# Optimization experiments

Measured on AMD Instinct MI355X. Metric: run time of the kernel, lower is better.

## Reference

```python
import jax, jax.numpy as jnp
import numpy as np

EPS = 1e-6


def _make_window_masks(nhw, nww, ws, shift):
    ph = jnp.arange(nhw).reshape(nhw, 1, 1, 1, 1, 1)
    pw = jnp.arange(nww).reshape(1, nww, 1, 1, 1, 1)
    qh = jnp.arange(ws).reshape(1, 1, ws, 1, 1, 1)
    qw = jnp.arange(ws).reshape(1, 1, 1, ws, 1, 1)
    kh = jnp.arange(ws).reshape(1, 1, 1, 1, ws, 1)
    kw = jnp.arange(ws).reshape(1, 1, 1, 1, 1, ws)
    top = ph == 0
    left = pw == 0
    qa = qh < shift
    ka = kh < shift
    ql = qw < shift
    kl = kw < shift
    m = ((left & top & (ql == kl) & (qa == ka))
         | (left & ~top & (ql == kl))
         | (~left & top & (qa == ka))
         | (~left & ~top))
    m = jnp.broadcast_to(m, (nhw, nww, ws, ws, ws, ws))
    return m.reshape(nhw, nww, ws * ws, ws * ws)


def _window(ws, x):
    # x: [b, nh, H, W, e] -> [b, nh, H//ws, W//ws, ws, ws, e]
    b, nh, H, W, e = x.shape
    x = x.reshape(b, nh, H // ws, ws, W // ws, ws, e)
    return jnp.transpose(x, (0, 1, 2, 4, 3, 5, 6))


def _unwindow(x):
    b, nh, h, w, wh, ww, e = x.shape
    x = jnp.transpose(x, (0, 1, 2, 4, 3, 5, 6))
    return x.reshape(b, nh, h * wh, w * ww, e)


def _rope_theta(pos, n_heads, d_head):
    # AxialRoPE: dim = d_head // 2, freqs [n_heads, dim//4]
    dim = d_head // 2
    freqs = jnp.exp(jnp.linspace(np.float32(np.log(np.pi)), np.float32(np.log(10.0 * np.pi)), n_heads * dim // 4 + 1)[:-1])
    freqs = freqs.reshape(dim // 4, n_heads).T  # [nh, dim//4]
    th = pos[..., None, 0:1] * freqs  # [b,H,W,nh,dim//4]
    tw = pos[..., None, 1:2] * freqs
    theta = jnp.concatenate([th, tw], axis=-1)  # [b,H,W,nh,d_head//4]
    return jnp.moveaxis(theta, -2, -4)  # [b,nh,H,W,d_head//4]


def _apply_rope(x, theta):
    # rotates first 2*d of head dim, pairs (i, i+d); rest passes through
    d = theta.shape[-1]
    x1, x2, rest = x[..., :d], x[..., d:2 * d], x[..., 2 * d:]
    cos, sin = jnp.cos(theta), jnp.sin(theta)
    y1 = x1 * cos - x2 * sin
    y2 = x2 * cos + x1 * sin
    return jnp.concatenate([y1, y2, rest], axis=-1)


def _forward(x, pos, cond, norm_scale, mod_w, mod_b, qkv_w, attn_scale, out_w, window_size, window_shift):
    b, H, W, d_model = x.shape
    n_heads = attn_scale.shape[0]
    d_head = d_model // n_heads
    ws, shift = window_size, window_shift
    skip = x
    # adaLN modulation: SiLU -> Linear(cond_features, 3*d_model)
    c = jax.nn.silu(cond) @ mod_w.T + mod_b  # [b, 3*d_model]
    sh, sc, gate = jnp.split(c, 3, axis=-1)
    # RMSNorm
    ms = jnp.mean(jnp.square(x.astype(jnp.float32)), axis=-1, keepdims=True)
    xn = x * (norm_scale * jax.lax.rsqrt(ms + EPS)).astype(x.dtype)
    # modulate
    xn = xn * (1.0 + sc[:, None, None, :]) + sh[:, None, None, :]
    # qkv projection: rearrange 'n h w (t nh e) -> t n nh h w e'
    qkv = (xn @ qkv_w.T).reshape(b, H, W, 3, n_heads, d_head)
    qkv = jnp.transpose(qkv, (3, 0, 4, 1, 2, 5))  # [3,b,nh,H,W,e]
    q, k, v = qkv[0], qkv[1], qkv[2]
    # cosine-sim QK scaling (per-head learned scale, eps 1e-6)
    sqrt_s = jnp.sqrt(attn_scale)[:, None, None, None]
    q = q * (sqrt_s * jax.lax.rsqrt(jnp.sum(jnp.square(q), -1, keepdims=True) + EPS))
    k = k * (sqrt_s * jax.lax.rsqrt(jnp.sum(jnp.square(k), -1, keepdims=True) + EPS))
    # axial RoPE
    theta = _rope_theta(pos, n_heads, d_head)
    q = _apply_rope(q, theta)
    k = _apply_rope(k, theta)
    # shifted-window attention with sdpa scale = 1.0
    def shift_win(t):
        return _window(ws, jnp.roll(t, (shift, shift), axis=(-3, -2)))
    h, w = H // ws, W // ws
    L = ws * ws
    qs = shift_win(q).reshape(b, n_heads, h, w, L, d_head)
    ks = shift_win(k).reshape(b, n_heads, h, w, L, d_head)
    vs = shift_win(v).reshape(b, n_heads, h, w, L, d_head)
    mask = _make_window_masks(h, w, ws, shift)  # [h,w,L,L] bool
    scores = jnp.einsum('bnhwqe,bnhwke->bnhwqk', qs, ks)
    scores = jnp.where(mask, scores, jnp.asarray(-1e9, scores.dtype))
    attn = jax.nn.softmax(scores, axis=-1)
    o = jnp.einsum('bnhwqk,bnhwke->bnhwqe', attn, vs)
    o = o.reshape(b, n_heads, h, w, ws, ws, d_head)
    o = jnp.roll(_unwindow(o), (-shift, -shift), axis=(-3, -2))  # [b,nh,H,W,e]
    o = jnp.transpose(o, (0, 2, 3, 1, 4)).reshape(b, H, W, d_model)
    o = o @ out_w.T
    return skip + gate[:, None, None, :] * o


def setup_inputs() -> dict:
    key = jax.random.key(0)
    ks = jax.random.split(key, 6)
    B, H, W, D, NH, CF = 2, 256, 256, 256, 4, 768
    x = jax.random.normal(ks[0], (B, H, W, D), jnp.float32)
    hh = jnp.linspace(-1.0, 1.0, H)
    ww = jnp.linspace(-1.0, 1.0, W)
    pos = jnp.stack(jnp.meshgrid(hh, ww, indexing='ij'), axis=-1)  # [H,W,2]
    pos = jnp.broadcast_to(pos, (B, H, W, 2)).astype(jnp.float32)
    cond = jax.random.normal(ks[1], (B, CF), jnp.float32)
    norm_scale = jnp.ones((D,), jnp.float32)
    mod_w = jax.random.normal(ks[2], (3 * D, CF), jnp.float32) * 0.02
    mod_b = jnp.zeros((3 * D,), jnp.float32)
    qkv_w = jax.random.normal(ks[3], (3 * D, D), jnp.float32) * (D ** -0.5)
    attn_scale = jnp.full((NH,), 10.0, jnp.float32)
    out_w = jax.random.normal(ks[4], (D, D), jnp.float32) * (D ** -0.5)
    return {"x": x, "pos": pos, "cond": cond, "norm_scale": norm_scale,
            "mod_w": mod_w, "mod_b": mod_b, "qkv_w": qkv_w,
            "attn_scale": attn_scale, "out_w": out_w,
            "window_size": 8, "window_shift": 4}


def reference(x, pos, cond, norm_scale, mod_w, mod_b, qkv_w, attn_scale, out_w, window_size, window_shift):
    return _forward(x, pos, cond, norm_scale, mod_w, mod_b, qkv_w, attn_scale, out_w, window_size, window_shift)
```

## Files before the change

### kernel.cpp

```cpp
#include <hip/hip_runtime.h>
#include <hip/hip_bf16.h>
#include <cstdint>

#define DEV __device__ __forceinline__

constexpr int D_   = 256;
constexpr int CF_  = 768;
constexpr int NTOK = 131072;
constexpr int SHIFT = 4;
constexpr float EPS_ = 1e-6f;
constexpr size_t PLANE = (size_t)NTOK * 64;

typedef short bf16x8 __attribute__((ext_vector_type(8)));
typedef float f32x4  __attribute__((ext_vector_type(4)));

DEV float bf2f(unsigned short u) {
    unsigned v = ((unsigned)u) << 16;
    return __builtin_bit_cast(float, v);
}
DEV unsigned short f2bf(float f) {
    unsigned u = __builtin_bit_cast(unsigned, f);
    unsigned r = (u + 0x7fffu + ((u >> 16) & 1u)) >> 16;
    return (unsigned short)r;
}
DEV unsigned cvtpk(float lo, float hi) {
    unsigned r;
    asm("v_cvt_pk_bf16_f32 %0, %1, %2" : "=v"(r) : "v"(lo), "v"(hi));
    return r;
}
DEV float wave_sum(float v) {
    #pragma unroll
    for (int o = 32; o; o >>= 1) v += __shfl_xor(v, o, 64);
    return v;
}
DEV void gl_lds16(const void* g, void* l) {
    __builtin_amdgcn_global_load_lds(
        (const __attribute__((address_space(1))) void*)g,
        (__attribute__((address_space(3))) void*)l, 16, 0, 0);
}

__global__ void k_mod(const float* __restrict__ cond, const float* __restrict__ mod_w,
                      const float* __restrict__ mod_b, float* __restrict__ c) {
    int wv = threadIdx.x >> 6, lane = threadIdx.x & 63;
    int idx = blockIdx.x * 4 + wv;
    int b = idx / (3 * D_), j = idx % (3 * D_);
    float acc = 0.f;
    for (int k = lane; k < CF_; k += 64) {
        float cv = cond[b * CF_ + k];
        float s = cv / (1.f + expf(-cv));
        acc += s * mod_w[(size_t)j * CF_ + k];
    }
    acc = wave_sum(acc);
    if (lane == 0) c[b * (3 * D_) + j] = acc + mod_b[j];
}

__global__ void k_prep(const float* __restrict__ x, const float* __restrict__ c,
                       const float* __restrict__ norm_scale,
                       const float* __restrict__ qkv_w, const float* __restrict__ out_w,
                       unsigned short* __restrict__ xnb,
                       unsigned short* __restrict__ qkvwb, unsigned short* __restrict__ outwb) {
    if (blockIdx.x < 32768) {
        int wv = threadIdx.x >> 6, lane = threadIdx.x & 63;
        int t = blockIdx.x * 4 + wv;
        int b = t >> 16;
        const float* xp = x + (size_t)t * D_ + lane * 4;
        float4 v = *(const float4*)xp;
        float s = v.x * v.x + v.y * v.y + v.z * v.z + v.w * v.w;
        s = wave_sum(s);
        float rinv = rsqrtf(s * (1.f / D_) + EPS_);
        float4 sc = *(const float4*)(c + b * 768 + 256 + lane * 4);
        float4 sh = *(const float4*)(c + b * 768 + lane * 4);
        float4 ns = *(const float4*)(norm_scale + lane * 4);
        float y0 = v.x * rinv * ((1.f + sc.x) * ns.x) + sh.x;
        float y1 = v.y * rinv * ((1.f + sc.y) * ns.y) + sh.y;
        float y2 = v.z * rinv * ((1.f + sc.z) * ns.z) + sh.z;
        float y3 = v.w * rinv * ((1.f + sc.w) * ns.w) + sh.w;
        uint2 p;
        p.x = cvtpk(y0, y1);
        p.y = cvtpk(y2, y3);
        *(uint2*)(xnb + (size_t)t * D_ + lane * 4) = p;
    } else {
        int i = (blockIdx.x - 32768) * 256 + threadIdx.x;
        const float* src; unsigned short* dst; int off;
        if (i < 49152) { src = qkv_w; dst = qkvwb; off = i * 4; }
        else           { src = out_w; dst = outwb; off = (i - 49152) * 4; }
        float4 v = *(const float4*)(src + off);
        uint2 p;
        p.x = cvtpk(v.x, v.y);
        p.y = cvtpk(v.z, v.w);
        *(uint2*)(dst + off) = p;
    }
}

__global__ __launch_bounds__(256) void k_qkv_mfma(const unsigned short* __restrict__ xnb,
                                                  const unsigned short* __restrict__ wb,
                                                  const float* __restrict__ attn_scale,
                                                  unsigned short* __restrict__ qkv) {
    __shared__ unsigned short SM[16384];
    unsigned short* As = SM;
    unsigned short* Bs = SM + 8192;
    const int t = threadIdx.x, l = t & 63, w = t >> 6;
    const int bid = blockIdx.x;
    const int lid = (bid & 7) * 768 + (bid >> 3);
    const int m0 = (lid / 6) * 128;
    const int nt = lid % 6;
    const int n0 = nt * 128;
    const int wm = w >> 1, wn = w & 1;
    f32x4 acc[4][4] = {};

    const int srow = w * 32 + (l >> 2);
    const int scol = (((l & 3) ^ ((l >> 3) & 3)) * 8);
    const unsigned short* aA = xnb + (size_t)(m0 + srow) * 256 + scol;
    const unsigned short* aB = wb  + (size_t)(n0 + srow) * 256 + scol;

    auto stage = [&](int buf, int k0) {
        gl_lds16(aA + k0,            &As[buf * 4096 + (w * 2 + 0) * 512]);
        gl_lds16(aA + k0 + 16 * 256, &As[buf * 4096 + (w * 2 + 1) * 512]);
        gl_lds16(aB + k0,            &Bs[buf * 4096 + (w * 2 + 0) * 512]);
        gl_lds16(aB + k0 + 16 * 256, &Bs[buf * 4096 + (w * 2 + 1) * 512]);
    };

    const int q16 = l & 15, g = l >> 4;
    const int rslot = (g ^ ((q16 >> 1) & 3)) * 8;

    stage(0, 0);
    int cur = 0;
    #pragma unroll
    for (int step = 0; step < 8; ++step) {
        if (step < 7) {
            stage(cur ^ 1, (step + 1) * 32);
            asm volatile("s_waitcnt vmcnt(4)" ::: "memory");
        } else {
            asm volatile("s_waitcnt vmcnt(0)" ::: "memory");
        }
        __builtin_amdgcn_s_barrier();
        __builtin_amdgcn_sched_barrier(0);
        bf16x8 af[4], bff[4];
        #pragma unroll
        for (int i = 0; i < 4; i++) {
            af[i]  = *(const bf16x8*)&As[cur * 4096 + (wm * 64 + i * 16 + q16) * 32 + rslot];
            bff[i] = *(const bf16x8*)&Bs[cur * 4096 + (wn * 64 + i * 16 + q16) * 32 + rslot];
        }
        #pragma unroll
        for (int i = 0; i < 4; i++)
            #pragma unroll
            for (int j = 0; j < 4; j++)
                acc[i][j] = __builtin_amdgcn_mfma_f32_16x16x32_bf16(af[i], bff[j], acc[i][j], 0, 0, 0);
        __builtin_amdgcn_sched_barrier(0);
        __builtin_amdgcn_s_barrier();
        cur ^= 1;
    }

    const int rl0 = wm * 64 + g * 4;

    if (nt < 4) {
        const int head = (nt * 2 + wn) & 3;
        const float ssc = sqrtf(attn_scale[head]);
        const float freq = expf(1.14472988584940017f + (float)((q16 & 7) * 4 + head) * 0.07195578545544534f);
        #pragma unroll
        for (int i = 0; i < 4; i++) {
            #pragma unroll
            for (int rg = 0; rg < 4; rg++) {
                float ss = acc[i][0][rg] * acc[i][0][rg] + acc[i][1][rg] * acc[i][1][rg]
                         + acc[i][2][rg] * acc[i][2][rg] + acc[i][3][rg] * acc[i][3][rg];
                ss += __shfl_xor(ss, 1, 64);
                ss += __shfl_xor(ss, 2, 64);
                ss += __shfl_xor(ss, 4, 64);
                ss += __shfl_xor(ss, 8, 64);
                const float rinv = ssc * rsqrtf(ss + EPS_);
                const int rl = rl0 + i * 16 + rg;
                const int row = m0 + rl;
                const int oy = (row >> 8) & 255, ox = row & 255;
                const float ph = -1.f + (float)oy * (2.f / 255.f);
                const float pw = -1.f + (float)ox * (2.f / 255.f);
                const float th = ((q16 < 8) ? ph : pw) * freq;
                float sn, cs;
                __sincosf(th, &sn, &cs);
                const float n0v = acc[i][0][rg] * rinv;
                const float n1v = acc[i][1][rg] * rinv;
                const float n2v = acc[i][2][rg] * rinv;
                const float n3v = acc[i][3][rg] * rinv;
                const int rx = rl & 15, wi = q16 & 7;
                float ov[4] = {n0v * cs - n1v * sn, n1v * cs + n0v * sn, n2v, n3v};
                #pragma unroll
                for (int jj = 0; jj < 4; jj++) {
                    const int slot = wn * 8 + 2 * jj + (q16 >> 3);
                    SM[rl * 128 + (slot ^ rx) * 8 + wi] = f2bf(ov[jj]);
                }
            }
        }
    } else {
        #pragma unroll
        for (int i = 0; i < 4; i++)
            #pragma unroll
            for (int rg = 0; rg < 4; rg++) {
                const int rl = rl0 + i * 16 + rg;
                const int rx = rl & 15, wi = q16 & 7;
                #pragma unroll
                for (int jj = 0; jj < 4; jj++) {
                    const int slot = wn * 8 + 2 * jj + (q16 >> 3);
                    SM[rl * 128 + (slot ^ rx) * 8 + wi] = f2bf(acc[i][jj][rg]);
                }
            }
    }
    __syncthreads();

    {
        const int s = t & 15, rr = t >> 4;
        const int colg = n0 + s * 8;
        const int plane = colg >> 6;
        const int ch = colg & 63;
        unsigned short* dstb = qkv + (size_t)plane * PLANE + ch;
        #pragma unroll
        for (int it = 0; it < 8; it++) {
            const int rl = rr + it * 16;
            uint4 vv = *(const uint4*)&SM[rl * 128 + (s ^ (rl & 15)) * 8];
            *(uint4*)(dstb + (size_t)(m0 + rl) * 64) = vv;
        }
    }
}

__global__ __launch_bounds__(256) void k_attn_out(const unsigned short* __restrict__ qkv,
                                                  const unsigned short* __restrict__ outwb,
                                                  const float* __restrict__ x,
                                                  const float* __restrict__ c,
                                                  float* __restrict__ out) {
    __shared__ unsigned short Mem[4 * 64 * 72];
    __shared__ float Ls[4][64];
    const int w = threadIdx.x >> 6, l = threadIdx.x & 63;
    const int bid = blockIdx.x;
    const int lid = (bid & 7) * 256 + (bid >> 3);
    const int wx = lid & 31, wy = (lid >> 5) & 31, b = lid >> 10;
    const int head = w;
    const int g = l >> 4, q16 = l & 15;
    unsigned short* Vt = &Mem[w * 4608];

    const unsigned short* qbase = qkv + (size_t)(0 + head) * PLANE;
    const unsigned short* kbase = qkv + (size_t)(4 + head) * PLANE;
    const unsigned short* vbase = qkv + (size_t)(8 + head) * PLANE;

    auto tokof = [&](int p) -> size_t {
        int oy = (wy * 8 + (p >> 3) - SHIFT) & 255;
        int ox = (wx * 8 + (p & 7) - SHIFT) & 255;
        return (size_t)b * 65536 + (size_t)oy * 256 + ox;
    };

    {
        const unsigned short* vp = vbase + tokof(l) * 64;
        uint4 vr[8];
        #pragma unroll
        for (int i = 0; i < 8; i++) vr[i] = *(const uint4*)(vp + i * 8);
        #pragma unroll
        for (int i = 0; i < 8; i++) {
            unsigned wd[4] = {vr[i].x, vr[i].y, vr[i].z, vr[i].w};
            #pragma unroll
            for (int cc = 0; cc < 4; cc++) {
                Vt[(i * 8 + cc * 2 + 0) * 72 + l] = (unsigned short)(wd[cc] & 0xffff);
                Vt[(i * 8 + cc * 2 + 1) * 72 + l] = (unsigned short)(wd[cc] >> 16);
            }
        }
    }

    bf16x8 af[4][2], bq[4][2];
    #pragma unroll
    for (int i = 0; i < 4; i++) {
        size_t tk = tokof(i * 16 + q16);
        const unsigned short* kp = kbase + tk * 64 + g * 8;
        af[i][0] = *(const bf16x8*)(kp);
        af[i][1] = *(const bf16x8*)(kp + 32);
        const unsigned short* qp = qbase + tk * 64 + g * 8;
        bq[i][0] = *(const bf16x8*)(qp);
        bq[i][1] = *(const bf16x8*)(qp + 32);
    }

    f32x4 st[4][4] = {};
    __builtin_amdgcn_s_setprio(1);
    #pragma unroll
    for (int ks = 0; ks < 2; ks++)
        #pragma unroll
        for (int i = 0; i < 4; i++)
            #pragma unroll
            for (int j = 0; j < 4; j++)
                st[i][j] = __builtin_amdgcn_mfma_f32_16x16x32_bf16(af[i][ks], bq[j][ks], st[i][j], 0, 0, 0);
    __builtin_amdgcn_s_setprio(0);

    const bool topw = (wy == 0), leftw = (wx == 0);
    if (topw || leftw) {
        #pragma unroll
        for (int j = 0; j < 4; j++) {
            int query = 16 * j + q16;
            bool qa = ((query >> 3) < 4), qlf = ((query & 7) < 4);
            #pragma unroll
            for (int i = 0; i < 4; i++)
                #pragma unroll
                for (int r = 0; r < 4; r++) {
                    int key = 16 * i + 4 * g + r;
                    bool ok = (!leftw || (qlf == ((key & 7) < 4))) &&
                              (!topw || (qa == ((key >> 3) < 4)));
                    if (!ok) st[i][j][r] = -1e9f;
                }
        }
    }

    #pragma unroll
    for (int j = 0; j < 4; j++) {
        float m = -1e30f;
        #pragma unroll
        for (int i = 0; i < 4; i++)
            #pragma unroll
            for (int r = 0; r < 4; r++) m = fmaxf(m, st[i][j][r]);
        m = fmaxf(m, __shfl_xor(m, 16, 64));
        m = fmaxf(m, __shfl_xor(m, 32, 64));
        float s = 0.f;
        #pragma unroll
        for (int i = 0; i < 4; i++)
            #pragma unroll
            for (int r = 0; r < 4; r++) {
                float p = __expf(st[i][j][r] - m);
                st[i][j][r] = p;
                s += p;
            }
        s += __shfl_xor(s, 16, 64);
        s += __shfl_xor(s, 32, 64);
        if (g == 0) Ls[w][16 * j + q16] = s;
    }

    bf16x8 vb[4][2];
    #pragma unroll
    for (int j = 0; j < 4; j++) {
        vb[j][0] = *(const bf16x8*)&Vt[(16 * j + q16) * 72 + g * 8];
        vb[j][1] = *(const bf16x8*)&Vt[(16 * j + q16) * 72 + 32 + g * 8];
    }
    const int ghi = g >> 1;
    const int srcl0 = ((2 * (g & 1)) & 3) * 16 + q16;
    const int srcl1 = ((2 * (g & 1) + 1) & 3) * 16 + q16;
    f32x4 o[4][4] = {};
    #pragma unroll
    for (int qb = 0; qb < 4; qb++) {
        unsigned pk[8];
        #pragma unroll
        for (int ih = 0; ih < 4; ih++) {
            pk[2 * ih]     = cvtpk(st[ih][qb][0], st[ih][qb][1]);
            pk[2 * ih + 1] = cvtpk(st[ih][qb][2], st[ih][qb][3]);
        }
        unsigned pw[8];
        #pragma unroll
        for (int ks = 0; ks < 2; ks++) {
            #pragma unroll
            for (int wd = 0; wd < 4; wd++) {
                const int srcl = (wd < 2) ? srcl0 : srcl1;
                unsigned va  = (unsigned)__shfl((int)pk[4 * ks + (wd & 1)], srcl, 64);
                unsigned vbb = (unsigned)__shfl((int)pk[4 * ks + 2 + (wd & 1)], srcl, 64);
                pw[ks * 4 + wd] = ghi ? vbb : va;
            }
        }
        uint4 paw0 = {pw[0], pw[1], pw[2], pw[3]};
        uint4 paw1 = {pw[4], pw[5], pw[6], pw[7]};
        bf16x8 paA = __builtin_bit_cast(bf16x8, paw0);
        bf16x8 paB = __builtin_bit_cast(bf16x8, paw1);
        __builtin_amdgcn_s_setprio(1);
        #pragma unroll
        for (int j = 0; j < 4; j++) {
            o[qb][j] = __builtin_amdgcn_mfma_f32_16x16x32_bf16(paA, vb[j][0], o[qb][j], 0, 0, 0);
            o[qb][j] = __builtin_amdgcn_mfma_f32_16x16x32_bf16(paB, vb[j][1], o[qb][j], 0, 0, 0);
        }
        __builtin_amdgcn_s_setprio(0);
    }

    __syncthreads();
    unsigned short* ost = Mem;
    #pragma unroll
    for (int i = 0; i < 4; i++) {
        float4 lv = *(const float4*)&Ls[w][16 * i + 4 * g];
        float lvr[4] = {lv.x, lv.y, lv.z, lv.w};
        #pragma unroll
        for (int r = 0; r < 4; r++) {
            const float invl = 1.f / lvr[r];
            const int row = 16 * i + 4 * g + r;
            #pragma unroll
            for (int j = 0; j < 4; j++)
                ost[row * 264 + head * 64 + 16 * j + q16] = f2bf(o[i][j][r] * invl);
        }
    }
    __syncthreads();

    f32x4 acc2[4][4] = {};
    #pragma unroll
    for (int ks = 0; ks < 8; ks++) {
        bf16x8 a2[4], b2[4];
        #pragma unroll
        for (int i = 0; i < 4; i++)
            a2[i] = *(const bf16x8*)&ost[(16 * i + q16) * 264 + ks * 32 + g * 8];
        #pragma unroll
        for (int j = 0; j < 4; j++)
            b2[j] = *(const bf16x8*)&outwb[(size_t)(w * 64 + 16 * j + q16) * 256 + ks * 32 + g * 8];
        __builtin_amdgcn_s_setprio(1);
        #pragma unroll
        for (int i = 0; i < 4; i++)
            #pragma unroll
            for (int j = 0; j < 4; j++)
                acc2[i][j] = __builtin_amdgcn_mfma_f32_16x16x32_bf16(a2[i], b2[j], acc2[i][j], 0, 0, 0);
        __builtin_amdgcn_s_setprio(0);
    }

    float gates[4];
    #pragma unroll
    for (int j = 0; j < 4; j++) gates[j] = c[b * 768 + 512 + w * 64 + 16 * j + q16];
    #pragma unroll
    for (int i = 0; i < 4; i++) {
        #pragma unroll
        for (int r = 0; r < 4; r++) {
            const int row = 16 * i + 4 * g + r;
            const size_t tok = tokof(row);
            float* op = out + tok * 256 + w * 64 + q16;
            const float* xp = x + tok * 256 + w * 64 + q16;
            #pragma unroll
            for (int j = 0; j < 4; j++)
                op[16 * j] = xp[16 * j] + gates[j] * acc2[i][j][r];
        }
    }
}

extern "C" void kernel_launch(void* const* d_in, const int* in_sizes, int n_in,
                              void* d_out, int out_size, void* d_ws, size_t ws_size,
                              hipStream_t stream) {
    const float* x          = (const float*)d_in[0];
    const float* cond       = (const float*)d_in[2];
    const float* norm_scale = (const float*)d_in[3];
    const float* mod_w      = (const float*)d_in[4];
    const float* mod_b      = (const float*)d_in[5];
    const float* qkv_w      = (const float*)d_in[6];
    const float* attn_scale = (const float*)d_in[7];
    const float* out_w      = (const float*)d_in[8];

    char* ws = (char*)d_ws;
    float* c               = (float*)ws;
    unsigned short* xnb    = (unsigned short*)(ws + 8192);
    unsigned short* qkvwb  = (unsigned short*)(ws + 8192 + 67108864);
    unsigned short* outwb  = (unsigned short*)(ws + 8192 + 67108864 + 393216);
    unsigned short* qkv    = (unsigned short*)(ws + 8192 + 67108864 + 524288);
    float* out             = (float*)d_out;

    hipLaunchKernelGGL(k_mod,  dim3(384),   dim3(256), 0, stream, cond, mod_w, mod_b, c);
    hipLaunchKernelGGL(k_prep, dim3(33024), dim3(256), 0, stream,
                       x, c, norm_scale, qkv_w, out_w, xnb, qkvwb, outwb);
    hipLaunchKernelGGL(k_qkv_mfma, dim3(6144), dim3(256), 0, stream, xnb, qkvwb, attn_scale, qkv);
    hipLaunchKernelGGL(k_attn_out, dim3(2048), dim3(256), 0, stream, qkv, outwb, x, c, out);
}
```

Baseline: 260.5 us.

## Split attention and output projection into separate kernels with tiled GEMM

```diff
diff --git a/kernel.cpp b/kernel.cpp
--- a/kernel.cpp
+++ b/kernel.cpp
@@ -220,11 +220,8 @@
     }
 }
 
-__global__ __launch_bounds__(256) void k_attn_out(const unsigned short* __restrict__ qkv,
-                                                  const unsigned short* __restrict__ outwb,
-                                                  const float* __restrict__ x,
-                                                  const float* __restrict__ c,
-                                                  float* __restrict__ out) {
+__global__ __launch_bounds__(256) void k_attn(const unsigned short* __restrict__ qkv,
+                                              unsigned short* __restrict__ obuf) {
     __shared__ unsigned short Mem[4 * 64 * 72];
     __shared__ float Ls[4][64];
     const int w = threadIdx.x >> 6, l = threadIdx.x & 63;
@@ -367,56 +364,99 @@
         __builtin_amdgcn_s_setprio(0);
     }
 
-    __syncthreads();
-    unsigned short* ost = Mem;
+    unsigned short* obase = obuf + (size_t)head * PLANE;
     #pragma unroll
     for (int i = 0; i < 4; i++) {
         float4 lv = *(const float4*)&Ls[w][16 * i + 4 * g];
         float lvr[4] = {lv.x, lv.y, lv.z, lv.w};
         #pragma unroll
         for (int r = 0; r < 4; r++) {
+            const int query = 16 * i + 4 * g + r;
             const float invl = 1.f / lvr[r];
-            const int row = 16 * i + 4 * g + r;
+            unsigned short* op = obase + tokof(query) * 64 + q16;
             #pragma unroll
             for (int j = 0; j < 4; j++)
-                ost[row * 264 + head * 64 + 16 * j + q16] = f2bf(o[i][j][r] * invl);
-        }
-    }
-    __syncthreads();
-
-    f32x4 acc2[4][4] = {};
-    #pragma unroll
-    for (int ks = 0; ks < 8; ks++) {
-        bf16x8 a2[4], b2[4];
-        #pragma unroll
-        for (int i = 0; i < 4; i++)
-            a2[i] = *(const bf16x8*)&ost[(16 * i + q16) * 264 + ks * 32 + g * 8];
-        #pragma unroll
-        for (int j = 0; j < 4; j++)
-            b2[j] = *(const bf16x8*)&outwb[(size_t)(w * 64 + 16 * j + q16) * 256 + ks * 32 + g * 8];
-        __builtin_amdgcn_s_setprio(1);
+                op[16 * j] = f2bf(o[i][j][r] * invl);
+        }
+    }
+}
+
+__global__ __launch_bounds__(256) void k_out_mfma(const unsigned short* __restrict__ obuf,
+                                                  const unsigned short* __restrict__ wb,
+                                                  const float* __restrict__ x,
+                                                  const float* __restrict__ c,
+                                                  float* __restrict__ out) {
+    __shared__ unsigned short As[2][4096];
+    __shared__ unsigned short Bs[2][4096];
+    const int t = threadIdx.x, l = t & 63, w = t >> 6;
+    const int bid = blockIdx.x;
+    const int lid = (bid & 7) * 256 + (bid >> 3);
+    const int m0 = (lid >> 1) * 128;
+    const int n0 = (lid & 1) * 128;
+    const int wm = w >> 1, wn = w & 1;
+    f32x4 acc[4][4] = {};
+
+    const int srow = w * 32 + (l >> 2);
+    const int scol = (((l & 3) ^ ((l >> 3) & 3)) * 8);
+    const unsigned short* aB = wb + (size_t)(n0 + srow) * 256 + scol;
+
+    auto stage = [&](int buf, int k0) {
+        const int colg = k0 + scol;
+        const unsigned short* aA = obuf + (size_t)(colg >> 6) * PLANE
+                                 + (size_t)(m0 + srow) * 64 + (colg & 63);
+        gl_lds16(aA,                 &As[buf][(w * 2 + 0) * 512]);
+        gl_lds16(aA + 16 * 64,       &As[buf][(w * 2 + 1) * 512]);
+        gl_lds16(aB + k0,            &Bs[buf][(w * 2 + 0) * 512]);
+        gl_lds16(aB + k0 + 16 * 256, &Bs[buf][(w * 2 + 1) * 512]);
+    };
+
+    const int q16 = l & 15, g = l >> 4;
+    const int rslot = (g ^ ((q16 >> 1) & 3)) * 8;
+
+    stage(0, 0);
+    int cur = 0;
+    #pragma unroll
+    for (int step = 0; step < 8; ++step) {
+        if (step < 7) {
+            stage(cur ^ 1, (step + 1) * 32);
+            asm volatile("s_waitcnt vmcnt(4)" ::: "memory");
+        } else {
+            asm volatile("s_waitcnt vmcnt(0)" ::: "memory");
+        }
+        __builtin_amdgcn_s_barrier();
+        __builtin_amdgcn_sched_barrier(0);
+        bf16x8 af[4], bff[4];
+        #pragma unroll
+        for (int i = 0; i < 4; i++) {
+            af[i]  = *(const bf16x8*)&As[cur][(wm * 64 + i * 16 + q16) * 32 + rslot];
+            bff[i] = *(const bf16x8*)&Bs[cur][(wn * 64 + i * 16 + q16) * 32 + rslot];
+        }
         #pragma unroll
         for (int i = 0; i < 4; i++)
             #pragma unroll
             for (int j = 0; j < 4; j++)
-                acc2[i][j] = __builtin_amdgcn_mfma_f32_16x16x32_bf16(a2[i], b2[j], acc2[i][j], 0, 0, 0);
-        __builtin_amdgcn_s_setprio(0);
-    }
-
+                acc[i][j] = __builtin_amdgcn_mfma_f32_16x16x32_bf16(af[i], bff[j], acc[i][j], 0, 0, 0);
+        __builtin_amdgcn_sched_barrier(0);
+        __builtin_amdgcn_s_barrier();
+        cur ^= 1;
+    }
+
+    const int row0 = m0 + wm * 64 + g * 4;
+    const int col0 = n0 + wn * 64 + q16;
+    const int b = m0 >> 16;
     float gates[4];
     #pragma unroll
-    for (int j = 0; j < 4; j++) gates[j] = c[b * 768 + 512 + w * 64 + 16 * j + q16];
+    for (int j = 0; j < 4; j++) gates[j] = c[b * 768 + 512 + col0 + j * 16];
     #pragma unroll
     for (int i = 0; i < 4; i++) {
         #pragma unroll
-        for (int r = 0; r < 4; r++) {
-            const int row = 16 * i + 4 * g + r;
-            const size_t tok = tokof(row);
-            float* op = out + tok * 256 + w * 64 + q16;
-            const float* xp = x + tok * 256 + w * 64 + q16;
+        for (int rg = 0; rg < 4; rg++) {
+            const int row = row0 + i * 16 + rg;
+            const float* xp = x + (size_t)row * 256 + col0;
+            float* op = out + (size_t)row * 256 + col0;
             #pragma unroll
             for (int j = 0; j < 4; j++)
-                op[16 * j] = xp[16 * j] + gates[j] * acc2[i][j][r];
+                op[j * 16] = xp[j * 16] + gates[j] * acc[i][j][rg];
         }
     }
 }
@@ -439,11 +479,13 @@
     unsigned short* qkvwb  = (unsigned short*)(ws + 8192 + 67108864);
     unsigned short* outwb  = (unsigned short*)(ws + 8192 + 67108864 + 393216);
     unsigned short* qkv    = (unsigned short*)(ws + 8192 + 67108864 + 524288);
+    unsigned short* obuf   = xnb;
     float* out             = (float*)d_out;
 
     hipLaunchKernelGGL(k_mod,  dim3(384),   dim3(256), 0, stream, cond, mod_w, mod_b, c);
     hipLaunchKernelGGL(k_prep, dim3(33024), dim3(256), 0, stream,
                        x, c, norm_scale, qkv_w, out_w, xnb, qkvwb, outwb);
     hipLaunchKernelGGL(k_qkv_mfma, dim3(6144), dim3(256), 0, stream, xnb, qkvwb, attn_scale, qkv);
-    hipLaunchKernelGGL(k_attn_out, dim3(2048), dim3(256), 0, stream, qkv, outwb, x, c, out);
-}
+    hipLaunchKernelGGL(k_attn, dim3(2048), dim3(256), 0, stream, qkv, obuf);
+    hipLaunchKernelGGL(k_out_mfma, dim3(2048), dim3(256), 0, stream, obuf, outwb, x, c, out);
+}
```

Measured after the change: 326.3 us. 25.2% more time.
